# Kernel tuning notes

Hardware: AMD Instinct MI355X
Metric: run time of the kernel (lower is better)

Reference implementation:

```python
import jax, jax.numpy as jnp
import numpy as np

N = 50000      # nodes
E = 800000     # edges (before self loops)
IN = 128       # in_channels
HID = 64       # hidden_channels
HEADS = 4      # num_heads
OUT = 40       # out_channels
NEG_SLOPE = 0.2


def setup_inputs() -> dict:
    key = jax.random.key(0)
    ks = jax.random.split(key, 16)
    x = jax.random.normal(ks[0], (N, IN), dtype=jnp.float32)
    edge_index = jax.random.randint(ks[1], (2, E), 0, N, dtype=jnp.int64)

    def lin(k, fan_in, fan_out):
        return jax.random.normal(k, (fan_in, fan_out), dtype=jnp.float32) * (1.0 / np.sqrt(fan_in))

    def att(k, h, c):
        return jax.random.normal(k, (h, c), dtype=jnp.float32) * (1.0 / np.sqrt(c))

    return {
        "x": x, "edge_index": edge_index,
        "W1": lin(ks[2], IN, HEADS * HID),
        "as1": att(ks[3], HEADS, HID), "ad1": att(ks[4], HEADS, HID),
        "b1": jnp.zeros((HEADS * HID,), jnp.float32),
        "W2": lin(ks[5], HEADS * HID, HEADS * HID),
        "as2": att(ks[6], HEADS, HID), "ad2": att(ks[7], HEADS, HID),
        "b2": jnp.zeros((HEADS * HID,), jnp.float32),
        "W3": lin(ks[8], HEADS * HID, OUT),
        "as3": att(ks[9], 1, OUT), "ad3": att(ks[10], 1, OUT),
        "b3": jnp.zeros((OUT,), jnp.float32),
    }


def _gat_layer(x, src, dst, W, a_src, a_dst, b):
    """One GATConv: linear -> per-edge attention -> segment softmax -> scatter-sum."""
    n = x.shape[0]
    H, C = a_src.shape
    h = (x @ W).reshape(n, H, C)                       # [N,H,C]
    al_s = jnp.einsum('nhc,hc->nh', h, a_src)          # [N,H]
    al_d = jnp.einsum('nhc,hc->nh', h, a_dst)          # [N,H]
    alpha = jax.nn.leaky_relu(al_s[src] + al_d[dst], NEG_SLOPE)  # [Etot,H]
    m = jax.ops.segment_max(alpha, dst, num_segments=n)          # stable softmax over incoming edges
    e = jnp.exp(alpha - m[dst])
    denom = jax.ops.segment_sum(e, dst, num_segments=n)
    attn = e / denom[dst]                              # [Etot,H]
    out = jax.ops.segment_sum(h[src] * attn[:, :, None], dst, num_segments=n)  # [N,H,C]
    return out.reshape(n, H * C) + b


def reference(x, edge_index, W1, as1, ad1, b1, W2, as2, ad2, b2, W3, as3, ad3, b3):
    # add self loops once (PyG GATConv default add_self_loops=True)
    loops = jnp.arange(N, dtype=edge_index.dtype)
    src = jnp.concatenate([edge_index[0], loops])
    dst = jnp.concatenate([edge_index[1], loops])

    h = _gat_layer(x, src, dst, W1, as1, ad1, b1)
    h = jax.nn.relu(h)                                 # dropout is identity in eval mode
    h = _gat_layer(h, src, dst, W2, as2, ad2, b2)
    h = jax.nn.relu(h)
    h = _gat_layer(h, src, dst, W3, as3, ad3, b3)      # final layer: 1 head
    return jax.nn.log_softmax(h, axis=-1)
```

## Files before the change

kernel.cpp:

```cpp
#include <hip/hip_runtime.h>
#include <math.h>

#define N_NODES 50000
#define N_EDGES 800000
#define ETOT    (N_EDGES + N_NODES)
#define EPAD_MAX 1200000
#define IN_CH   128
#define OUT_CH  40
#define NEG     0.2f
#define CAP     64

#define P1   32
#define NPC  1563
#define CCAP 34000
#define P2   16
#define NPF  98
#define NFINE (P1 * P2)
#define FCAP 2400

typedef __attribute__((ext_vector_type(8))) short bf16x8;
typedef __attribute__((ext_vector_type(4))) float f32x4;
typedef __attribute__((ext_vector_type(2))) float f32x2;

__device__ inline unsigned short f2bf(float f) {
    unsigned int u = __float_as_uint(f);
    return (unsigned short)((u + 0x7FFFu + ((u >> 16) & 1u)) >> 16);
}
__device__ inline float bf2f(unsigned short u) {
    return __uint_as_float((unsigned int)u << 16);
}
__device__ inline float lrelu(float a) { return (a > 0.f) ? a : NEG * a; }

__global__ __launch_bounds__(256) void k_b1(const int* __restrict__ ei,
                                            int* __restrict__ ccur,
                                            unsigned int* __restrict__ cbuf) {
    __shared__ int lcnt[P1], lbase[P1], lcur[P1];
    int tid = threadIdx.x;
    if (tid < P1) lcnt[tid] = 0;
    __syncthreads();
    for (int i = blockIdx.x * 256 + tid; i < ETOT; i += 256 * 256) {
        int d = (i < N_EDGES) ? ei[N_EDGES + i] : (i - N_EDGES);
        atomicAdd(&lcnt[d / NPC], 1);
    }
    __syncthreads();
    if (tid < P1) {
        lbase[tid] = atomicAdd(&ccur[tid], lcnt[tid]);
        lcur[tid] = 0;
    }
    __syncthreads();
    for (int i = blockIdx.x * 256 + tid; i < ETOT; i += 256 * 256) {
        int s, d;
        if (i < N_EDGES) { s = ei[i]; d = ei[N_EDGES + i]; }
        else             { s = i - N_EDGES; d = s; }
        int p = d / NPC;
        int off = atomicAdd(&lcur[p], 1);
        cbuf[(long)p * CCAP + lbase[p] + off] = (unsigned int)s | ((unsigned int)d << 16);
    }
}

__global__ __launch_bounds__(256) void k_b2(const int* __restrict__ ccur,
                                            const unsigned int* __restrict__ cbuf,
                                            int* __restrict__ fcur,
                                            unsigned int* __restrict__ fbuf) {
    __shared__ int lcnt[P2], lbase[P2], lcur2[P2];
    int c = blockIdx.x >> 3;
    int sub = blockIdx.x & 7;
    int tid = threadIdx.x;
    int n = ccur[c];
    if (tid < P2) lcnt[tid] = 0;
    __syncthreads();
    int base = c * NPC;
    for (int i = sub * 256 + tid; i < n; i += 8 * 256) {
        int d = (int)(cbuf[(long)c * CCAP + i] >> 16);
        atomicAdd(&lcnt[(d - base) / NPF], 1);
    }
    __syncthreads();
    if (tid < P2) {
        lbase[tid] = atomicAdd(&fcur[c * P2 + tid], lcnt[tid]);
        lcur2[tid] = 0;
    }
    __syncthreads();
    for (int i = sub * 256 + tid; i < n; i += 8 * 256) {
        unsigned int u = cbuf[(long)c * CCAP + i];
        int d = (int)(u >> 16);
        int j = (d - base) / NPF;
        int off = atomicAdd(&lcur2[j], 1);
        fbuf[(long)(c * P2 + j) * FCAP + lbase[j] + off] = u;
    }
}

__global__ __launch_bounds__(256) void k_deg(const int* __restrict__ fcur,
                                             const unsigned int* __restrict__ fbuf,
                                             int* __restrict__ deg) {
    __shared__ int cnt[NPF];
    int f = blockIdx.x;
    int tid = threadIdx.x;
    int c = f >> 4, j = f & 15;
    int n0 = c * NPC + j * NPF;
    int nend = min(min(n0 + NPF, (c + 1) * NPC), N_NODES);
    if (tid < NPF) cnt[tid] = 0;
    __syncthreads();
    int n = fcur[f];
    for (int i = tid; i < n; i += 256)
        atomicAdd(&cnt[(int)(fbuf[(long)f * FCAP + i] >> 16) - n0], 1);
    __syncthreads();
    if (tid < NPF && n0 + tid < nend) deg[n0 + tid] = cnt[tid];
}

__global__ void k_scan1(const int* __restrict__ deg, int* __restrict__ start,
                        int* __restrict__ bsum) {
    __shared__ int sh[256];
    int tid = threadIdx.x;
    int i = blockIdx.x * 256 + tid;
    int v = (i < N_NODES) ? ((deg[i] + 7) & ~7) : 0;
    int x = v;
    sh[tid] = x;
    __syncthreads();
    #pragma unroll
    for (int off = 1; off < 256; off <<= 1) {
        int t = (tid >= off) ? sh[tid - off] : 0;
        __syncthreads();
        x += t;
        sh[tid] = x;
        __syncthreads();
    }
    if (i < N_NODES) start[i] = x - v;
    if (tid == 255) bsum[blockIdx.x] = x;
}

__global__ void k_scan2(int* __restrict__ bsum, int nb) {
    __shared__ int sh[256];
    int tid = threadIdx.x;
    int v = (tid < nb) ? bsum[tid] : 0;
    int x = v;
    sh[tid] = x;
    __syncthreads();
    #pragma unroll
    for (int off = 1; off < 256; off <<= 1) {
        int t = (tid >= off) ? sh[tid - off] : 0;
        __syncthreads();
        x += t;
        sh[tid] = x;
        __syncthreads();
    }
    if (tid < nb) bsum[tid] = x - v;
}

__global__ void k_scan3(int* __restrict__ start, const int* __restrict__ bsum) {
    int i = blockIdx.x * 256 + threadIdx.x;
    if (i < N_NODES) start[i] += bsum[blockIdx.x];
}

__global__ __launch_bounds__(256) void k_scat(const int* __restrict__ fcur,
                                              const unsigned int* __restrict__ fbuf,
                                              const int* __restrict__ start,
                                              int* __restrict__ eSrc) {
    __shared__ int offs[NPF];
    int f = blockIdx.x;
    int tid = threadIdx.x;
    int c = f >> 4, j = f & 15;
    int n0 = c * NPC + j * NPF;
    int nend = min(min(n0 + NPF, (c + 1) * NPC), N_NODES);
    if (tid < NPF && n0 + tid < nend) offs[tid] = start[n0 + tid];
    __syncthreads();
    int n = fcur[f];
    for (int i = tid; i < n; i += 256) {
        unsigned int u = fbuf[(long)f * FCAP + i];
        int d = (int)(u >> 16);
        int pos = atomicAdd(&offs[d - n0], 1);
        eSrc[pos] = (int)(u & 0xFFFFu);
    }
}

__global__ void k_wt_all(const float* __restrict__ W1, const float* __restrict__ W2,
                         const float* __restrict__ W3,
                         unsigned short* __restrict__ Wt1,
                         unsigned short* __restrict__ Wt2,
                         unsigned short* __restrict__ Wt3) {
    int i = blockIdx.x * blockDim.x + threadIdx.x;
    if (i < 32768) {
        int n = i >> 7, k = i & 127;
        Wt1[i] = f2bf(W1[(long)k * 256 + n]);
    } else if (i < 98304) {
        int j = i - 32768;
        int n = j >> 8, k = j & 255;
        Wt2[j] = f2bf(W2[(long)k * 256 + n]);
    } else if (i < 114688) {
        int j = i - 98304;
        int n = j >> 8, k = j & 255;
        Wt3[j] = (n < OUT_CH) ? f2bf(W3[(long)k * OUT_CH + n]) : (unsigned short)0;
    }
}

#define PITCH 40
template<int BN, int FM, int FN, bool CVT, bool FP8OUT>
__global__ __launch_bounds__(256) void k_mfma(const void* __restrict__ Araw,
                                              const unsigned short* __restrict__ Bt,
                                              void* __restrict__ Cout,
                                              int M, int K, int Ncol) {
    __shared__ unsigned short As[128 * PITCH];
    __shared__ unsigned short Bs[BN * PITCH];
    const int WCOLS = BN / (FN * 16);
    int tid = threadIdx.x;
    int wave = tid >> 6, lane = tid & 63;
    int quad = lane >> 4, l16 = lane & 15;
    int wr = wave / WCOLS, wc = wave % WCOLS;
    long row0 = (long)blockIdx.x * 128;
    int col0 = blockIdx.y * BN;

    f32x4 acc[FM][FN] = {};

    for (int k0 = 0; k0 < K; k0 += 32) {
        for (int c = tid; c < 512; c += 256) {
            int r = c >> 2, kp = (c & 3) << 3;
            long gr = row0 + r;
            if (CVT) {
                const float* A32 = (const float*)Araw;
                ushort4 lo = {0,0,0,0}, hi = {0,0,0,0};
                if (gr < M) {
                    float4 v0 = *(const float4*)(A32 + gr * K + k0 + kp);
                    float4 v1 = *(const float4*)(A32 + gr * K + k0 + kp + 4);
                    lo.x = f2bf(v0.x); lo.y = f2bf(v0.y); lo.z = f2bf(v0.z); lo.w = f2bf(v0.w);
                    hi.x = f2bf(v1.x); hi.y = f2bf(v1.y); hi.z = f2bf(v1.z); hi.w = f2bf(v1.w);
                }
                *(ushort4*)(As + r * PITCH + kp) = lo;
                *(ushort4*)(As + r * PITCH + kp + 4) = hi;
            } else {
                const unsigned short* A16 = (const unsigned short*)Araw;
                uint4 v = {0u, 0u, 0u, 0u};
                if (gr < M) v = *(const uint4*)(A16 + gr * K + k0 + kp);
                *(uint4*)(As + r * PITCH + kp) = v;
            }
        }
        for (int c = tid; c < BN * 4; c += 256) {
            int r = c >> 2, kp = (c & 3) << 3;
            uint4 v = *(const uint4*)(Bt + (long)(col0 + r) * K + k0 + kp);
            *(uint4*)(Bs + r * PITCH + kp) = v;
        }
        __syncthreads();
        bf16x8 af[FM], bfr[FN];
        #pragma unroll
        for (int i = 0; i < FM; ++i)
            af[i] = *(const bf16x8*)(As + (wr * FM * 16 + i * 16 + l16) * PITCH + quad * 8);
        #pragma unroll
        for (int j = 0; j < FN; ++j)
            bfr[j] = *(const bf16x8*)(Bs + (wc * FN * 16 + j * 16 + l16) * PITCH + quad * 8);
        #pragma unroll
        for (int i = 0; i < FM; ++i)
            #pragma unroll
            for (int j = 0; j < FN; ++j)
                acc[i][j] = __builtin_amdgcn_mfma_f32_16x16x32_bf16(af[i], bfr[j], acc[i][j], 0, 0, 0);
        __syncthreads();
    }

    if (FP8OUT) {
        unsigned char* C8 = (unsigned char*)Cout;
        #pragma unroll
        for (int i = 0; i < FM; ++i) {
            #pragma unroll
            for (int v = 0; v < 4; ++v) {
                long row = row0 + wr * FM * 16 + i * 16 + quad * 4 + v;
                if (row < M) {
                    int p01 = __builtin_amdgcn_cvt_pk_fp8_f32(acc[i][0][v], acc[i][1][v], 0, false);
                    int p23 = __builtin_amdgcn_cvt_pk_fp8_f32(acc[i][2][v], acc[i][3][v], 0, false);
                    unsigned char* b = C8 + row * 256 + col0 + wc * (FN * 16) + l16;
                    b[0]  = (unsigned char)(p01 & 0xFF);
                    b[16] = (unsigned char)((p01 >> 8) & 0xFF);
                    b[32] = (unsigned char)(p23 & 0xFF);
                    b[48] = (unsigned char)((p23 >> 8) & 0xFF);
                }
            }
        }
    } else {
        unsigned short* C = (unsigned short*)Cout;
        #pragma unroll
        for (int i = 0; i < FM; ++i) {
            long rowb = row0 + wr * FM * 16 + i * 16 + quad * 4;
            #pragma unroll
            for (int j = 0; j < FN; ++j) {
                int col = col0 + wc * FN * 16 + j * 16 + l16;
                if (col < Ncol) {
                    #pragma unroll
                    for (int v = 0; v < 4; ++v) {
                        long r = rowb + v;
                        if (r < M) C[r * Ncol + col] = f2bf(acc[i][j][v]);
                    }
                }
            }
        }
    }
}

__global__ __launch_bounds__(256) void k_logits4(const unsigned char* __restrict__ h8,
                                                 const float* __restrict__ a_s,
                                                 const float* __restrict__ a_d,
                                                 float* __restrict__ als,
                                                 float* __restrict__ ald) {
    int wave = (blockIdx.x * blockDim.x + threadIdx.x) >> 6;
    int lane = threadIdx.x & 63;
    if (wave >= N_NODES) return;
    unsigned int hu = *(const unsigned int*)(h8 + (long)wave * 256 + lane * 4);
    f32x2 lo = __builtin_amdgcn_cvt_pk_f32_fp8((int)hu, false);
    f32x2 hi = __builtin_amdgcn_cvt_pk_f32_fp8((int)hu, true);
    int head = lane >> 4;
    int cbase = (lane * 4) & 63;
    float4 sv = *(const float4*)(a_s + head * 64 + cbase);
    float4 dv = *(const float4*)(a_d + head * 64 + cbase);
    float ps = lo.x * sv.x + lo.y * sv.y + hi.x * sv.z + hi.y * sv.w;
    float pd = lo.x * dv.x + lo.y * dv.y + hi.x * dv.z + hi.y * dv.w;
    #pragma unroll
    for (int off = 1; off < 16; off <<= 1) {
        ps += __shfl_xor(ps, off);
        pd += __shfl_xor(pd, off);
    }
    if ((lane & 15) == 0) {
        als[wave * 4 + head] = ps;
        ald[wave * 4 + head] = pd;
    }
}

__global__ __launch_bounds__(256) void k_logits1(const unsigned short* __restrict__ h,
                                                 const float* __restrict__ a_s,
                                                 const float* __restrict__ a_d,
                                                 float* __restrict__ als,
                                                 float* __restrict__ ald) {
    int wave = (blockIdx.x * blockDim.x + threadIdx.x) >> 6;
    int lane = threadIdx.x & 63;
    if (wave >= N_NODES) return;
    float hv = (lane < OUT_CH) ? bf2f(h[(long)wave * OUT_CH + lane]) : 0.f;
    float ps = (lane < OUT_CH) ? hv * a_s[lane] : 0.f;
    float pd = (lane < OUT_CH) ? hv * a_d[lane] : 0.f;
    #pragma unroll
    for (int off = 1; off < 64; off <<= 1) {
        ps += __shfl_xor(ps, off);
        pd += __shfl_xor(pd, off);
    }
    if (lane == 0) {
        als[wave] = ps;
        ald[wave] = pd;
    }
}

__global__ __launch_bounds__(256) void k_agg4(const unsigned char* __restrict__ h8,
                                              const int* __restrict__ start,
                                              const int* __restrict__ deg,
                                              const int* __restrict__ eSrc,
                                              const float* __restrict__ als,
                                              const float* __restrict__ ald,
                                              const float* __restrict__ bias,
                                              unsigned short* __restrict__ out) {
    __shared__ float wbuf[4][CAP * 4];
    __shared__ int   sbuf[4][CAP];
    int wid = threadIdx.x >> 6;
    int node = (blockIdx.x * blockDim.x + threadIdx.x) >> 6;
    int lane = threadIdx.x & 63;
    if (node >= N_NODES) return;
    int st = start[node];
    int dgp = (deg[node] + 7) & ~7;
    const int* ep = eSrc + st;

    int l16 = lane & 15, headw = lane >> 4;
    float aldd4 = ald[node * 4 + headw];
    int ncap = (dgp < CAP) ? dgp : CAP;
    for (int c = 0; c < ncap; c += 16) {
        int slot = c + l16;
        bool ok = (slot < ncap);
        int raw = ok ? ep[slot] : -1;
        int ss = (raw < 0) ? 0 : raw;
        float a = als[(long)ss * 4 + headw] + aldd4;
        float w = (raw < 0) ? 0.f : __expf(lrelu(a));
        if (ok) {
            wbuf[wid][slot * 4 + headw] = w;
            if (headw == 0) sbuf[wid][slot] = ss;
        }
    }

    int half = lane >> 5;
    int hl = lane & 31;
    int head8 = hl >> 3;
    float den = 0.f;
    float acc[8] = {};

    int ncpair = ncap >> 1;
    int jA = 0, jB = ncpair - 4;

    auto do_pairs = [&](int p0, int p1, int p2, int p3) {
        int slot[4] = {p0 * 2 + half, p1 * 2 + half, p2 * 2 + half, p3 * 2 + half};
        int s[4];
        float w[4];
        #pragma unroll
        for (int u = 0; u < 4; ++u) {
            s[u] = sbuf[wid][slot[u]];
            w[u] = wbuf[wid][slot[u] * 4 + head8];
        }
        uint2 hv[4];
        #pragma unroll
        for (int u = 0; u < 4; ++u)
            hv[u] = *(const uint2*)(h8 + (long)s[u] * 256 + hl * 8);
        #pragma unroll
        for (int u = 0; u < 4; ++u) {
            den += w[u];
            f32x2 p0v = __builtin_amdgcn_cvt_pk_f32_fp8((int)hv[u].x, false);
            f32x2 p1v = __builtin_amdgcn_cvt_pk_f32_fp8((int)hv[u].x, true);
            f32x2 p2v = __builtin_amdgcn_cvt_pk_f32_fp8((int)hv[u].y, false);
            f32x2 p3v = __builtin_amdgcn_cvt_pk_f32_fp8((int)hv[u].y, true);
            acc[0] += w[u] * p0v.x;
            acc[1] += w[u] * p0v.y;
            acc[2] += w[u] * p1v.x;
            acc[3] += w[u] * p1v.y;
            acc[4] += w[u] * p2v.x;
            acc[5] += w[u] * p2v.y;
            acc[6] += w[u] * p3v.x;
            acc[7] += w[u] * p3v.y;
        }
    };

    while (jA < jB) {
        do_pairs(jA, jA + 1, jB, jB + 1);
        do_pairs(jA + 2, jA + 3, jB + 2, jB + 3);
        jA += 4; jB -= 4;
    }
    if (jA == jB) {
        do_pairs(jA, jA + 1, jA + 2, jA + 3);
    }

    if (dgp > ncap) {
        float aldd8 = ald[node * 4 + head8];
        for (int j = ncap; j < dgp; j += 2) {
            int raw = ep[j + half];
            int ss = (raw < 0) ? 0 : raw;
            float w = (raw < 0) ? 0.f : __expf(lrelu(als[(long)ss * 4 + head8] + aldd8));
            uint2 hv = *(const uint2*)(h8 + (long)ss * 256 + hl * 8);
            f32x2 p0v = __builtin_amdgcn_cvt_pk_f32_fp8((int)hv.x, false);
            f32x2 p1v = __builtin_amdgcn_cvt_pk_f32_fp8((int)hv.x, true);
            f32x2 p2v = __builtin_amdgcn_cvt_pk_f32_fp8((int)hv.y, false);
            f32x2 p3v = __builtin_amdgcn_cvt_pk_f32_fp8((int)hv.y, true);
            den += w;
            acc[0] += w * p0v.x;
            acc[1] += w * p0v.y;
            acc[2] += w * p1v.x;
            acc[3] += w * p1v.y;
            acc[4] += w * p2v.x;
            acc[5] += w * p2v.y;
            acc[6] += w * p3v.x;
            acc[7] += w * p3v.y;
        }
    }

    den += __shfl_xor(den, 32);
    #pragma unroll
    for (int c = 0; c < 8; ++c) acc[c] += __shfl_xor(acc[c], 32);

    if (half == 0) {
        float inv = 1.f / den;
        int cb = hl * 8;
        float4 b0 = *(const float4*)(bias + cb);
        float4 b1 = *(const float4*)(bias + cb + 4);
        float v0 = fmaxf(acc[0] * inv + b0.x, 0.f);
        float v1 = fmaxf(acc[1] * inv + b0.y, 0.f);
        float v2 = fmaxf(acc[2] * inv + b0.z, 0.f);
        float v3 = fmaxf(acc[3] * inv + b0.w, 0.f);
        float v4 = fmaxf(acc[4] * inv + b1.x, 0.f);
        float v5 = fmaxf(acc[5] * inv + b1.y, 0.f);
        float v6 = fmaxf(acc[6] * inv + b1.z, 0.f);
        float v7 = fmaxf(acc[7] * inv + b1.w, 0.f);
        uint4 o;
        o.x = (unsigned int)f2bf(v0) | ((unsigned int)f2bf(v1) << 16);
        o.y = (unsigned int)f2bf(v2) | ((unsigned int)f2bf(v3) << 16);
        o.z = (unsigned int)f2bf(v4) | ((unsigned int)f2bf(v5) << 16);
        o.w = (unsigned int)f2bf(v6) | ((unsigned int)f2bf(v7) << 16);
        *(uint4*)(out + (long)node * 256 + cb) = o;
    }
}

__global__ __launch_bounds__(256) void k_agg1(const unsigned short* __restrict__ h,
                                              const int* __restrict__ start,
                                              const int* __restrict__ deg,
                                              const int* __restrict__ eSrc,
                                              const float* __restrict__ als,
                                              const float* __restrict__ ald,
                                              const float* __restrict__ bias,
                                              float* __restrict__ out) {
    int node = (blockIdx.x * blockDim.x + threadIdx.x) >> 6;
    int lane = threadIdx.x & 63;
    if (node >= N_NODES) return;
    int q = lane >> 4, r = lane & 15;
    bool act = (r < 10);
    int st = start[node];
    int dgp = (deg[node] + 7) & ~7;
    const int* ep = eSrc + st;
    float aldd = ald[node];

    float den = 0.f;
    float4 acc = {0.f, 0.f, 0.f, 0.f};

    int j = 0;
    for (; j + 16 <= dgp; j += 16) {
        int base = j + q * 4;
        int s[4];
        float w[4];
        #pragma unroll
        for (int u = 0; u < 4; ++u) s[u] = ep[base + u];
        #pragma unroll
        for (int u = 0; u < 4; ++u) {
            int raw = s[u];
            int ss = (raw < 0) ? 0 : raw;
            w[u] = (raw < 0) ? 0.f : __expf(lrelu(als[ss] + aldd));
            s[u] = ss;
        }
        ushort4 hh[4];
        #pragma unroll
        for (int u = 0; u < 4; ++u) {
            ushort4 t = {0, 0, 0, 0};
            if (act) t = *(const ushort4*)(h + (long)s[u] * OUT_CH + r * 4);
            hh[u] = t;
        }
        #pragma unroll
        for (int u = 0; u < 4; ++u) {
            den += w[u];
            acc.x += w[u] * bf2f(hh[u].x);
            acc.y += w[u] * bf2f(hh[u].y);
            acc.z += w[u] * bf2f(hh[u].z);
            acc.w += w[u] * bf2f(hh[u].w);
        }
    }
    if (j < dgp) {
        int base = j + q * 2;
        int s[2];
        float w[2];
        #pragma unroll
        for (int u = 0; u < 2; ++u) s[u] = ep[base + u];
        #pragma unroll
        for (int u = 0; u < 2; ++u) {
            int raw = s[u];
            int ss = (raw < 0) ? 0 : raw;
            w[u] = (raw < 0) ? 0.f : __expf(lrelu(als[ss] + aldd));
            s[u] = ss;
        }
        ushort4 hh[2];
        #pragma unroll
        for (int u = 0; u < 2; ++u) {
            ushort4 t = {0, 0, 0, 0};
            if (act) t = *(const ushort4*)(h + (long)s[u] * OUT_CH + r * 4);
            hh[u] = t;
        }
        #pragma unroll
        for (int u = 0; u < 2; ++u) {
            den += w[u];
            acc.x += w[u] * bf2f(hh[u].x);
            acc.y += w[u] * bf2f(hh[u].y);
            acc.z += w[u] * bf2f(hh[u].z);
            acc.w += w[u] * bf2f(hh[u].w);
        }
    }

    #pragma unroll
    for (int off = 16; off < 64; off <<= 1) {
        acc.x += __shfl_xor(acc.x, off);
        acc.y += __shfl_xor(acc.y, off);
        acc.z += __shfl_xor(acc.z, off);
        acc.w += __shfl_xor(acc.w, off);
        den   += __shfl_xor(den, off);
    }
    float inv = 1.f / den;
    float4 bv = {0.f, 0.f, 0.f, 0.f};
    if (act) bv = *(const float4*)(bias + r * 4);
    float4 v;
    v.x = acc.x * inv + bv.x;
    v.y = acc.y * inv + bv.y;
    v.z = acc.z * inv + bv.z;
    v.w = acc.w * inv + bv.w;
    float mx = act ? fmaxf(fmaxf(v.x, v.y), fmaxf(v.z, v.w)) : -INFINITY;
    #pragma unroll
    for (int off = 1; off < 16; off <<= 1) mx = fmaxf(mx, __shfl_xor(mx, off));
    float sum = act ? (__expf(v.x - mx) + __expf(v.y - mx) + __expf(v.z - mx) + __expf(v.w - mx)) : 0.f;
    #pragma unroll
    for (int off = 1; off < 16; off <<= 1) sum += __shfl_xor(sum, off);
    float lse = mx + logf(sum);
    if (q == 0 && act) {
        float4 o;
        o.x = v.x - lse;
        o.y = v.y - lse;
        o.z = v.z - lse;
        o.w = v.w - lse;
        *(float4*)(out + (long)node * OUT_CH + r * 4) = o;
    }
}

extern "C" void kernel_launch(void* const* d_in, const int* in_sizes, int n_in,
                              void* d_out, int out_size, void* d_ws, size_t ws_size,
                              hipStream_t stream) {
    (void)in_sizes; (void)n_in; (void)out_size; (void)ws_size;
    const float* x   = (const float*)d_in[0];
    const int*   ei  = (const int*)d_in[1];
    const float* W1  = (const float*)d_in[2];
    const float* as1 = (const float*)d_in[3];
    const float* ad1 = (const float*)d_in[4];
    const float* b1  = (const float*)d_in[5];
    const float* W2  = (const float*)d_in[6];
    const float* as2 = (const float*)d_in[7];
    const float* ad2 = (const float*)d_in[8];
    const float* b2  = (const float*)d_in[9];
    const float* W3  = (const float*)d_in[10];
    const float* as3 = (const float*)d_in[11];
    const float* ad3 = (const float*)d_in[12];
    const float* b3  = (const float*)d_in[13];
    float* out = (float*)d_out;

    char* p = (char*)d_ws;
    auto alloc = [&](size_t b) { char* r = p; p += (b + 255) & ~(size_t)255; return r; };
    int*   deg   = (int*)alloc((size_t)N_NODES * 4);
    int*   start = (int*)alloc((size_t)N_NODES * 4);
    int*   bsum  = (int*)alloc(256 * 4);
    int*   ccur  = (int*)alloc((size_t)P1 * 4);
    int*   fcur  = (int*)alloc((size_t)NFINE * 4);
    unsigned int* cbuf = (unsigned int*)alloc((size_t)P1 * CCAP * 4);
    unsigned int* fbuf = (unsigned int*)alloc((size_t)NFINE * FCAP * 4);
    int*   eSrc  = (int*)alloc((size_t)EPAD_MAX * 4);
    float* als   = (float*)alloc((size_t)N_NODES * 4 * 4);
    float* ald   = (float*)alloc((size_t)N_NODES * 4 * 4);
    unsigned char*  hA8  = (unsigned char*)alloc((size_t)N_NODES * 256);
    unsigned short* hBbf = (unsigned short*)alloc((size_t)N_NODES * 256 * 2);
    unsigned short* h3bf = (unsigned short*)alloc((size_t)N_NODES * OUT_CH * 2);
    unsigned short* Wt1  = (unsigned short*)alloc((size_t)256 * IN_CH * 2);
    unsigned short* Wt2  = (unsigned short*)alloc((size_t)256 * 256 * 2);
    unsigned short* Wt3  = (unsigned short*)alloc((size_t)64 * 256 * 2);

    const int NB = (N_NODES + 255) / 256;
    const int WB = (N_NODES + 3) / 4;
    const int MB = (N_NODES + 127) / 128;

    hipMemsetAsync(ccur, 0, (size_t)P1 * 4, stream);
    hipMemsetAsync(fcur, 0, (size_t)NFINE * 4, stream);
    hipMemsetAsync(eSrc, 0xFF, (size_t)EPAD_MAX * 4, stream);
    k_b1<<<256, 256, 0, stream>>>(ei, ccur, cbuf);
    k_b2<<<256, 256, 0, stream>>>(ccur, cbuf, fcur, fbuf);
    k_deg<<<NFINE, 256, 0, stream>>>(fcur, fbuf, deg);
    k_scan1<<<NB, 256, 0, stream>>>(deg, start, bsum);
    k_scan2<<<1, 256, 0, stream>>>(bsum, NB);
    k_scan3<<<NB, 256, 0, stream>>>(start, bsum);
    k_scat<<<NFINE, 256, 0, stream>>>(fcur, fbuf, start, eSrc);

    k_wt_all<<<448, 256, 0, stream>>>(W1, W2, W3, Wt1, Wt2, Wt3);

    k_mfma<128, 4, 4, true, true><<<dim3(MB, 2), 256, 0, stream>>>(x, Wt1, hA8, N_NODES, IN_CH, 256);
    k_logits4<<<WB, 256, 0, stream>>>(hA8, as1, ad1, als, ald);
    k_agg4<<<WB, 256, 0, stream>>>(hA8, start, deg, eSrc, als, ald, b1, hBbf);

    k_mfma<128, 4, 4, false, true><<<dim3(MB, 2), 256, 0, stream>>>(hBbf, Wt2, hA8, N_NODES, 256, 256);
    k_logits4<<<WB, 256, 0, stream>>>(hA8, as2, ad2, als, ald);
    k_agg4<<<WB, 256, 0, stream>>>(hA8, start, deg, eSrc, als, ald, b2, hBbf);

    k_mfma<64, 2, 4, false, false><<<dim3(MB, 1), 256, 0, stream>>>(hBbf, Wt3, h3bf, N_NODES, 256, OUT_CH);
    k_logits1<<<WB, 256, 0, stream>>>(h3bf, as3, ad3, als, ald);
    k_agg1<<<WB, 256, 0, stream>>>(h3bf, start, deg, eSrc, als, ald, b3, out);
}
```

Baseline: 351.3 us.

## Fuse attention logits into MFMA epilogue, merge scan kernels, drop eSrc memset

Computes the per-node source/destination attention logits directly from the MFMA accumulators in the GEMM epilogue, which removes the three separate logits kernels and their re-read of the projected features. Merges the second and third scan passes by having every block redo the small block-sum scan, and replaces the full 0xFF memset of the padded edge array with per-node pad filling inside the scatter kernel. It also packs the fp8 aggregation accumulators into float2 vectors so the compiler can use packed FMA. Logits are now taken from unrounded fp32 accumulators rather than fp8/bf16-rounded features, which slightly changes numerics. The padding region past the last real node is no longer initialised.

After: 321.0 us. 8.6% less time.

```diff
diff --git a/kernel.cpp b/kernel.cpp
--- a/kernel.cpp
+++ b/kernel.cpp
@@ -128,8 +128,10 @@
     if (tid == 255) bsum[blockIdx.x] = x;
 }
 
-__global__ void k_scan2(int* __restrict__ bsum, int nb) {
+__global__ void k_scan3(int* __restrict__ start, const int* __restrict__ bsum,
+                        int nb) {
     __shared__ int sh[256];
+    __shared__ int ex[256];
     int tid = threadIdx.x;
     int v = (tid < nb) ? bsum[tid] : 0;
     int x = v;
@@ -143,12 +145,11 @@
         sh[tid] = x;
         __syncthreads();
     }
-    if (tid < nb) bsum[tid] = x - v;
-}
-
-__global__ void k_scan3(int* __restrict__ start, const int* __restrict__ bsum) {
-    int i = blockIdx.x * 256 + threadIdx.x;
-    if (i < N_NODES) start[i] += bsum[blockIdx.x];
+    ex[tid] = x - v;
+    __syncthreads();
+    int add = ex[blockIdx.x];
+    int i = blockIdx.x * 256 + tid;
+    if (i < N_NODES) start[i] += add;
 }
 
 __global__ __launch_bounds__(256) void k_scat(const int* __restrict__ fcur,
@@ -156,12 +157,18 @@
                                               const int* __restrict__ start,
                                               int* __restrict__ eSrc) {
     __shared__ int offs[NPF];
+    __shared__ int base[NPF];
     int f = blockIdx.x;
     int tid = threadIdx.x;
     int c = f >> 4, j = f & 15;
     int n0 = c * NPC + j * NPF;
     int nend = min(min(n0 + NPF, (c + 1) * NPC), N_NODES);
-    if (tid < NPF && n0 + tid < nend) offs[tid] = start[n0 + tid];
+    int nn = nend - n0;
+    if (tid < NPF && tid < nn) {
+        int b = start[n0 + tid];
+        offs[tid] = b;
+        base[tid] = b;
+    }
     __syncthreads();
     int n = fcur[f];
     for (int i = tid; i < n; i += 256) {
@@ -169,6 +176,13 @@
         int d = (int)(u >> 16);
         int pos = atomicAdd(&offs[d - n0], 1);
         eSrc[pos] = (int)(u & 0xFFFFu);
+    }
+    __syncthreads();
+    if (tid < NPF && tid < nn) {
+        int endp = offs[tid];
+        int dg = endp - base[tid];
+        int stop = base[tid] + ((dg + 7) & ~7);
+        for (int k2 = endp; k2 < stop; ++k2) eSrc[k2] = -1;
     }
 }
 
@@ -193,10 +207,14 @@
 }
 
 #define PITCH 40
-template<int BN, int FM, int FN, bool CVT, bool FP8OUT>
+template<int BN, int FM, int FN, bool CVT, bool FP8OUT, bool L4>
 __global__ __launch_bounds__(256) void k_mfma(const void* __restrict__ Araw,
                                               const unsigned short* __restrict__ Bt,
                                               void* __restrict__ Cout,
+                                              const float* __restrict__ a_s,
+                                              const float* __restrict__ a_d,
+                                              float* __restrict__ als,
+                                              float* __restrict__ ald,
                                               int M, int K, int Ncol) {
     __shared__ unsigned short As[128 * PITCH];
     __shared__ unsigned short Bs[BN * PITCH];
@@ -253,6 +271,44 @@
         __syncthreads();
     }
 
+    {
+        int head = L4 ? (blockIdx.y * WCOLS + wc) : 0;
+        float as_v[FN], ad_v[FN];
+        #pragma unroll
+        for (int j = 0; j < FN; ++j) {
+            int cidx = j * 16 + l16;
+            if (L4) {
+                as_v[j] = a_s[head * 64 + cidx];
+                ad_v[j] = a_d[head * 64 + cidx];
+            } else {
+                as_v[j] = (cidx < OUT_CH) ? a_s[cidx] : 0.f;
+                ad_v[j] = (cidx < OUT_CH) ? a_d[cidx] : 0.f;
+            }
+        }
+        #pragma unroll
+        for (int i = 0; i < FM; ++i) {
+            #pragma unroll
+            for (int v = 0; v < 4; ++v) {
+                float ps = acc[i][0][v] * as_v[0] + acc[i][1][v] * as_v[1]
+                         + acc[i][2][v] * as_v[2] + acc[i][3][v] * as_v[3];
+                float pd = acc[i][0][v] * ad_v[0] + acc[i][1][v] * ad_v[1]
+                         + acc[i][2][v] * ad_v[2] + acc[i][3][v] * ad_v[3];
+                #pragma unroll
+                for (int off = 1; off < 16; off <<= 1) {
+                    ps += __shfl_xor(ps, off);
+                    pd += __shfl_xor(pd, off);
+                }
+                if (l16 == 0) {
+                    long row = row0 + wr * (FM * 16) + i * 16 + quad * 4 + v;
+                    if (row < M) {
+                        if (L4) { als[row * 4 + head] = ps; ald[row * 4 + head] = pd; }
+                        else    { als[row] = ps; ald[row] = pd; }
+                    }
+                }
+            }
+        }
+    }
+
     if (FP8OUT) {
         unsigned char* C8 = (unsigned char*)Cout;
         #pragma unroll
@@ -288,56 +344,6 @@
                 }
             }
         }
-    }
-}
-
-__global__ __launch_bounds__(256) void k_logits4(const unsigned char* __restrict__ h8,
-                                                 const float* __restrict__ a_s,
-                                                 const float* __restrict__ a_d,
-                                                 float* __restrict__ als,
-                                                 float* __restrict__ ald) {
-    int wave = (blockIdx.x * blockDim.x + threadIdx.x) >> 6;
-    int lane = threadIdx.x & 63;
-    if (wave >= N_NODES) return;
-    unsigned int hu = *(const unsigned int*)(h8 + (long)wave * 256 + lane * 4);
-    f32x2 lo = __builtin_amdgcn_cvt_pk_f32_fp8((int)hu, false);
-    f32x2 hi = __builtin_amdgcn_cvt_pk_f32_fp8((int)hu, true);
-    int head = lane >> 4;
-    int cbase = (lane * 4) & 63;
-    float4 sv = *(const float4*)(a_s + head * 64 + cbase);
-    float4 dv = *(const float4*)(a_d + head * 64 + cbase);
-    float ps = lo.x * sv.x + lo.y * sv.y + hi.x * sv.z + hi.y * sv.w;
-    float pd = lo.x * dv.x + lo.y * dv.y + hi.x * dv.z + hi.y * dv.w;
-    #pragma unroll
-    for (int off = 1; off < 16; off <<= 1) {
-        ps += __shfl_xor(ps, off);
-        pd += __shfl_xor(pd, off);
-    }
-    if ((lane & 15) == 0) {
-        als[wave * 4 + head] = ps;
-        ald[wave * 4 + head] = pd;
-    }
-}
-
-__global__ __launch_bounds__(256) void k_logits1(const unsigned short* __restrict__ h,
-                                                 const float* __restrict__ a_s,
-                                                 const float* __restrict__ a_d,
-                                                 float* __restrict__ als,
-                                                 float* __restrict__ ald) {
-    int wave = (blockIdx.x * blockDim.x + threadIdx.x) >> 6;
-    int lane = threadIdx.x & 63;
-    if (wave >= N_NODES) return;
-    float hv = (lane < OUT_CH) ? bf2f(h[(long)wave * OUT_CH + lane]) : 0.f;
-    float ps = (lane < OUT_CH) ? hv * a_s[lane] : 0.f;
-    float pd = (lane < OUT_CH) ? hv * a_d[lane] : 0.f;
-    #pragma unroll
-    for (int off = 1; off < 64; off <<= 1) {
-        ps += __shfl_xor(ps, off);
-        pd += __shfl_xor(pd, off);
-    }
-    if (lane == 0) {
-        als[wave] = ps;
-        ald[wave] = pd;
     }
 }
 
@@ -379,7 +385,7 @@
     int hl = lane & 31;
     int head8 = hl >> 3;
     float den = 0.f;
-    float acc[8] = {};
+    f32x2 acc2[4] = {};
 
     int ncpair = ncap >> 1;
     int jA = 0, jB = ncpair - 4;
@@ -400,18 +406,11 @@
         #pragma unroll
         for (int u = 0; u < 4; ++u) {
             den += w[u];
-            f32x2 p0v = __builtin_amdgcn_cvt_pk_f32_fp8((int)hv[u].x, false);
-            f32x2 p1v = __builtin_amdgcn_cvt_pk_f32_fp8((int)hv[u].x, true);
-            f32x2 p2v = __builtin_amdgcn_cvt_pk_f32_fp8((int)hv[u].y, false);
-            f32x2 p3v = __builtin_amdgcn_cvt_pk_f32_fp8((int)hv[u].y, true);
-            acc[0] += w[u] * p0v.x;
-            acc[1] += w[u] * p0v.y;
-            acc[2] += w[u] * p1v.x;
-            acc[3] += w[u] * p1v.y;
-            acc[4] += w[u] * p2v.x;
-            acc[5] += w[u] * p2v.y;
-            acc[6] += w[u] * p3v.x;
-            acc[7] += w[u] * p3v.y;
+            f32x2 w2; w2.x = w[u]; w2.y = w[u];
+            acc2[0] += w2 * __builtin_amdgcn_cvt_pk_f32_fp8((int)hv[u].x, false);
+            acc2[1] += w2 * __builtin_amdgcn_cvt_pk_f32_fp8((int)hv[u].x, true);
+            acc2[2] += w2 * __builtin_amdgcn_cvt_pk_f32_fp8((int)hv[u].y, false);
+            acc2[3] += w2 * __builtin_amdgcn_cvt_pk_f32_fp8((int)hv[u].y, true);
         }
     };
 
@@ -431,39 +430,35 @@
             int ss = (raw < 0) ? 0 : raw;
             float w = (raw < 0) ? 0.f : __expf(lrelu(als[(long)ss * 4 + head8] + aldd8));
             uint2 hv = *(const uint2*)(h8 + (long)ss * 256 + hl * 8);
-            f32x2 p0v = __builtin_amdgcn_cvt_pk_f32_fp8((int)hv.x, false);
-            f32x2 p1v = __builtin_amdgcn_cvt_pk_f32_fp8((int)hv.x, true);
-            f32x2 p2v = __builtin_amdgcn_cvt_pk_f32_fp8((int)hv.y, false);
-            f32x2 p3v = __builtin_amdgcn_cvt_pk_f32_fp8((int)hv.y, true);
             den += w;
-            acc[0] += w * p0v.x;
-            acc[1] += w * p0v.y;
-            acc[2] += w * p1v.x;
-            acc[3] += w * p1v.y;
-            acc[4] += w * p2v.x;
-            acc[5] += w * p2v.y;
-            acc[6] += w * p3v.x;
-            acc[7] += w * p3v.y;
+            f32x2 w2; w2.x = w; w2.y = w;
+            acc2[0] += w2 * __builtin_amdgcn_cvt_pk_f32_fp8((int)hv.x, false);
+            acc2[1] += w2 * __builtin_amdgcn_cvt_pk_f32_fp8((int)hv.x, true);
+            acc2[2] += w2 * __builtin_amdgcn_cvt_pk_f32_fp8((int)hv.y, false);
+            acc2[3] += w2 * __builtin_amdgcn_cvt_pk_f32_fp8((int)hv.y, true);
         }
     }
 
     den += __shfl_xor(den, 32);
     #pragma unroll
-    for (int c = 0; c < 8; ++c) acc[c] += __shfl_xor(acc[c], 32);
+    for (int c = 0; c < 4; ++c) {
+        acc2[c].x += __shfl_xor(acc2[c].x, 32);
+        acc2[c].y += __shfl_xor(acc2[c].y, 32);
+    }
 
     if (half == 0) {
         float inv = 1.f / den;
         int cb = hl * 8;
         float4 b0 = *(const float4*)(bias + cb);
         float4 b1 = *(const float4*)(bias + cb + 4);
-        float v0 = fmaxf(acc[0] * inv + b0.x, 0.f);
-        float v1 = fmaxf(acc[1] * inv + b0.y, 0.f);
-        float v2 = fmaxf(acc[2] * inv + b0.z, 0.f);
-        float v3 = fmaxf(acc[3] * inv + b0.w, 0.f);
-        float v4 = fmaxf(acc[4] * inv + b1.x, 0.f);
-        float v5 = fmaxf(acc[5] * inv + b1.y, 0.f);
-        float v6 = fmaxf(acc[6] * inv + b1.z, 0.f);
-        float v7 = fmaxf(acc[7] * inv + b1.w, 0.f);
+        float v0 = fmaxf(acc2[0].x * inv + b0.x, 0.f);
+        float v1 = fmaxf(acc2[0].y * inv + b0.y, 0.f);
+        float v2 = fmaxf(acc2[1].x * inv + b0.z, 0.f);
+        float v3 = fmaxf(acc2[1].y * inv + b0.w, 0.f);
+        float v4 = fmaxf(acc2[2].x * inv + b1.x, 0.f);
+        float v5 = fmaxf(acc2[2].y * inv + b1.y, 0.f);
+        float v6 = fmaxf(acc2[3].x * inv + b1.z, 0.f);
+        float v7 = fmaxf(acc2[3].y * inv + b1.w, 0.f);
         uint4 o;
         o.x = (unsigned int)f2bf(v0) | ((unsigned int)f2bf(v1) << 16);
         o.y = (unsigned int)f2bf(v2) | ((unsigned int)f2bf(v3) << 16);
@@ -612,8 +607,7 @@
     int*   deg   = (int*)alloc((size_t)N_NODES * 4);
     int*   start = (int*)alloc((size_t)N_NODES * 4);
     int*   bsum  = (int*)alloc(256 * 4);
-    int*   ccur  = (int*)alloc((size_t)P1 * 4);
-    int*   fcur  = (int*)alloc((size_t)NFINE * 4);
+    int*   cnts  = (int*)alloc((size_t)(P1 + NFINE) * 4);
     unsigned int* cbuf = (unsigned int*)alloc((size_t)P1 * CCAP * 4);
     unsigned int* fbuf = (unsigned int*)alloc((size_t)NFINE * FCAP * 4);
     int*   eSrc  = (int*)alloc((size_t)EPAD_MAX * 4);
@@ -625,33 +619,32 @@
     unsigned short* Wt1  = (unsigned short*)alloc((size_t)256 * IN_CH * 2);
     unsigned short* Wt2  = (unsigned short*)alloc((size_t)256 * 256 * 2);
     unsigned short* Wt3  = (unsigned short*)alloc((size_t)64 * 256 * 2);
+    int* ccur = cnts;
+    int* fcur = cnts + P1;
 
     const int NB = (N_NODES + 255) / 256;
     const int WB = (N_NODES + 3) / 4;
     const int MB = (N_NODES + 127) / 128;
 
-    hipMemsetAsync(ccur, 0, (size_t)P1 * 4, stream);
-    hipMemsetAsync(fcur, 0, (size_t)NFINE * 4, stream);
-    hipMemsetAsync(eSrc, 0xFF, (size_t)EPAD_MAX * 4, stream);
+    hipMemsetAsync(cnts, 0, (size_t)(P1 + NFINE) * 4, stream);
     k_b1<<<256, 256, 0, stream>>>(ei, ccur, cbuf);
     k_b2<<<256, 256, 0, stream>>>(ccur, cbuf, fcur, fbuf);
     k_deg<<<NFINE, 256, 0, stream>>>(fcur, fbuf, deg);
     k_scan1<<<NB, 256, 0, stream>>>(deg, start, bsum);
-    k_scan2<<<1, 256, 0, stream>>>(bsum, NB);
-    k_scan3<<<NB, 256, 0, stream>>>(start, bsum);
+    k_scan3<<<NB, 256, 0, stream>>>(start, bsum, NB);
     k_scat<<<NFINE, 256, 0, stream>>>(fcur, fbuf, start, eSrc);
 
     k_wt_all<<<448, 256, 0, stream>>>(W1, W2, W3, Wt1, Wt2, Wt3);
 
-    k_mfma<128, 4, 4, true, true><<<dim3(MB, 2), 256, 0, stream>>>(x, Wt1, hA8, N_NODES, IN_CH, 256);
-    k_logits4<<<WB, 256, 0, stream>>>(hA8, as1, ad1, als, ald);
+    k_mfma<128, 4, 4, true, true, true><<<dim3(MB, 2), 256, 0, stream>>>(
+        x, Wt1, hA8, as1, ad1, als, ald, N_NODES, IN_CH, 256);
     k_agg4<<<WB, 256, 0, stream>>>(hA8, start, deg, eSrc, als, ald, b1, hBbf);
 
-    k_mfma<128, 4, 4, false, true><<<dim3(MB, 2), 256, 0, stream>>>(hBbf, Wt2, hA8, N_NODES, 256, 256);
-    k_logits4<<<WB, 256, 0, stream>>>(hA8, as2, ad2, als, ald);
+    k_mfma<128, 4, 4, false, true, true><<<dim3(MB, 2), 256, 0, stream>>>(
+        hBbf, Wt2, hA8, as2, ad2, als, ald, N_NODES, 256, 256);
     k_agg4<<<WB, 256, 0, stream>>>(hA8, start, deg, eSrc, als, ald, b2, hBbf);
 
-    k_mfma<64, 2, 4, false, false><<<dim3(MB, 1), 256, 0, stream>>>(hBbf, Wt3, h3bf, N_NODES, 256, OUT_CH);
-    k_logits1<<<WB, 256, 0, stream>>>(h3bf, as3, ad3, als, ald);
+    k_mfma<64, 2, 4, false, false, false><<<dim3(MB, 1), 256, 0, stream>>>(
+        hBbf, Wt3, h3bf, as3, ad3, als, ald, N_NODES, 256, OUT_CH);
     k_agg1<<<WB, 256, 0, stream>>>(h3bf, start, deg, eSrc, als, ald, b3, out);
 }
```
